# Performance work log

Hardware: AMD Instinct MI355X
Metric: run time of the kernel (lower is better)

Reference implementation:

```python
import jax, jax.numpy as jnp
import numpy as np

W = H = 64
CONFIGS = [(1, 3), (2, 3), (3, 3)]  # (dilation, kernel_size)
OUT_PER_CFG = 32
IN_CH = 32


def build_mask():
    # One (W+1, H+1) mask per config, broadcast over (out, in) channels.
    masks = []
    for d, k in CONFIGS:
        m = np.zeros((W + 1, H + 1), dtype=np.float32)
        k1 = (k - 1) * (d - 1) + k  # effective dilated kernel extent
        s1 = (W - k1) // 2 + 1
        e1 = (W + k1) // 2 + 1
        s2 = (H - k1) // 2 + 1
        e2 = (H + k1) // 2 + 1
        m[s1:e1:d, s2:e2:d] = 1.0
        masks.append(np.broadcast_to(m, (OUT_PER_CFG, 1, W + 1, H + 1)))
    return jnp.asarray(np.concatenate(masks, axis=0))  # (96, 1, 65, 65)


def setup_inputs() -> dict:
    key = jax.random.key(0)
    k1, k2 = jax.random.split(key)
    x = jax.random.normal(k1, (16, IN_CH, W, H), dtype=jnp.float32)
    # small init so tanh does not saturate
    weight = jax.random.normal(k2, (OUT_PER_CFG * len(CONFIGS), IN_CH, W + 1, H + 1), dtype=jnp.float32) * 0.01
    mask = build_mask()
    gamma = jnp.ones((OUT_PER_CFG * len(CONFIGS),), dtype=jnp.float32)
    beta = jnp.zeros((OUT_PER_CFG * len(CONFIGS),), dtype=jnp.float32)
    return {"x": x, "weight": weight, "mask": mask, "gamma": gamma, "beta": beta}


def reference(x, weight, mask, gamma, beta):
    # circular pad: last dim by H//2 each side, dim -2 by W//2 each side
    xp = jnp.pad(x, ((0, 0), (0, 0), (W // 2, W // 2), (H // 2, H // 2)), mode="wrap")
    y = jax.lax.conv_general_dilated(
        xp, weight * mask,
        window_strides=(1, 1), padding="VALID",
        dimension_numbers=("NCHW", "OIHW", "NCHW"),
    )  # (B, 96, 64, 64)
    # BatchNorm2d in training mode: batch statistics over (N, H, W), eps=1e-5
    mean = jnp.mean(y, axis=(0, 2, 3))
    var = jnp.var(y, axis=(0, 2, 3))
    yn = (y - mean[None, :, None, None]) * jax.lax.rsqrt(var + 1e-5)[None, :, None, None]
    yn = yn * gamma[None, :, None, None] + beta[None, :, None, None]
    return jnp.tanh(yn)
```

## Files before the change

### kernel.cpp

```cpp
#include <hip/hip_runtime.h>
#include <math.h>

#define BATCH 16
#define CIN 32
#define COUT 96
#define WH 64
#define IMG (WH*WH)
#define NPIX (BATCH*IMG)
#define PWELEMS (3*9*32*32)
#define XTELEMS (BATCH*IMG*CIN)
#define NBLK 768
#define NGRP 96
#define PAD 16
#define ZWORDS (4*NGRP*PAD + PAD)

typedef __attribute__((ext_vector_type(8))) short short8;
typedef __attribute__((ext_vector_type(4))) float floatx4;

__device__ __forceinline__ unsigned short f2bf(float f) {
    union { float f; unsigned u; } v; v.f = f;
    unsigned r = v.u + 0x7FFFu + ((v.u >> 16) & 1u);
    return (unsigned short)(r >> 16);
}
__device__ __forceinline__ float bf2f(unsigned short u) {
    union { unsigned u; float f; } v; v.u = (unsigned)u << 16; return v.f;
}

#define GLDS(src, dst) __builtin_amdgcn_global_load_lds( \
    (const __attribute__((address_space(1))) void*)(src), \
    (__attribute__((address_space(3))) void*)(dst), 16, 0, 0)

__device__ __forceinline__ float fast_tanh(float xv) {
    float e = __expf(2.0f * xv);
    return fmaf(-2.0f, __builtin_amdgcn_rcpf(e + 1.0f), 1.0f);
}

__global__ __launch_bounds__(256) void prep_kernel(
    const float* __restrict__ x, const float* __restrict__ w,
    unsigned short* __restrict__ xT, unsigned short* __restrict__ pw,
    unsigned* __restrict__ zbase)
{
    int blk = blockIdx.x;
    if (blk < 512) {
        int gid  = blk * 256 + threadIdx.x;
        int pt   = gid >> 1;
        int half = gid & 1;
        int b    = pt >> 12;
        int pix  = pt & 4095;
        const float* xb = x + ((size_t)b * CIN + half * 16) * IMG + pix;
        unsigned packed[8];
#pragma unroll
        for (int c2 = 0; c2 < 8; c2++) {
            unsigned short lo = f2bf(xb[(size_t)(2 * c2) * IMG]);
            unsigned short hi = f2bf(xb[(size_t)(2 * c2 + 1) * IMG]);
            packed[c2] = (unsigned)lo | ((unsigned)hi << 16);
        }
        uint4* dst = (uint4*)(xT + (size_t)pt * 32 + half * 16);
        dst[0] = make_uint4(packed[0], packed[1], packed[2], packed[3]);
        dst[1] = make_uint4(packed[4], packed[5], packed[6], packed[7]);
    } else if (blk < 620) {
        int e = (blk - 512) * 256 + threadIdx.x;
        if (e >= PWELEMS) return;
        int cfg = e / (9 * 1024);
        int rem = e % (9 * 1024);
        int tap = rem >> 10;
        int oc  = (rem >> 5) & 31;
        int c   = rem & 31;
        int d   = cfg + 1;
        int du  = tap / 3, dv = tap % 3;
        size_t idx = (((size_t)(cfg * 32 + oc) * CIN + c) * 65 + (32 + (du - 1) * d)) * 65
                     + (32 + (dv - 1) * d);
        pw[e] = f2bf(w[idx]);
    } else {
        for (int i = threadIdx.x; i < ZWORDS; i += 256) zbase[i] = 0u;
    }
}

__global__ __launch_bounds__(256, 3) void conv_bn_kernel(
    const unsigned short* __restrict__ xT, const unsigned short* __restrict__ pw,
    float* __restrict__ gsum, float* __restrict__ gsq,
    unsigned* __restrict__ gcnt, unsigned* __restrict__ ggo,
    unsigned* __restrict__ groot,
    const float* __restrict__ gamma, const float* __restrict__ beta,
    float* __restrict__ out)
{
    __shared__ __align__(16) unsigned short tile[10 * 2048];
    __shared__ float red_s[4][32];
    __shared__ float red_q[4][32];
    __shared__ float sc_a[32];
    __shared__ float sc_b[32];

    int bid  = blockIdx.x;
    int rowg = bid & 15;
    int rest = bid >> 4;
    int cfg  = rest % 3;
    int b    = rest / 3;
    int d    = cfg + 1;
    int i0   = rowg * 4;

    int t    = threadIdx.x;
    int wv   = t >> 6;
    int lane = t & 63;
    int l15  = lane & 15;
    int quad = lane >> 4;

    const unsigned short* xTb = xT + (size_t)b * IMG * 32;
#pragma unroll
    for (int rr = 0; rr < 10; rr++) {
        int gi = (i0 - 3 + rr) & 63;
        GLDS(xTb + (size_t)gi * 2048 + t * 8, &tile[rr * 2048 + t * 8]);
    }

    const unsigned short* pwc = pw + (size_t)cfg * 9 * 32 * 32;
    short8 af[2][9];
#pragma unroll
    for (int h = 0; h < 2; h++)
#pragma unroll
        for (int tap = 0; tap < 9; tap++)
            af[h][tap] = *(const short8*)(pwc + ((tap * 32 + h * 16 + l15) * 32 + quad * 8));

    float gam = 0.f, bet = 0.f;
    if (t < 32) { gam = gamma[cfg * 32 + t]; bet = beta[cfg * 32 + t]; }

    __syncthreads();

    float ss[2][4], qq[2][4];
#pragma unroll
    for (int h = 0; h < 2; h++)
#pragma unroll
        for (int r = 0; r < 4; r++) { ss[h][r] = 0.f; qq[h][r] = 0.f; }

    unsigned ypk[2][4][2];
    int row = i0 + wv;

#pragma unroll
    for (int cgi = 0; cgi < 4; cgi++) {
        floatx4 a0 = {0.f, 0.f, 0.f, 0.f};
        floatx4 a1 = {0.f, 0.f, 0.f, 0.f};
#pragma unroll
        for (int du = 0; du < 3; du++) {
            int rowloc = wv + 3 + (du - 1) * d;
            const unsigned short* rbase = &tile[rowloc * 2048 + quad * 8];
#pragma unroll
            for (int dv = 0; dv < 3; dv++) {
                int col = (cgi * 16 + l15 + (dv - 1) * d) & 63;
                short8 bf = *(const short8*)(rbase + col * 32);
                a0 = __builtin_amdgcn_mfma_f32_16x16x32_bf16(af[0][du * 3 + dv], bf, a0, 0, 0, 0);
                a1 = __builtin_amdgcn_mfma_f32_16x16x32_bf16(af[1][du * 3 + dv], bf, a1, 0, 0, 0);
            }
        }
#pragma unroll
        for (int r = 0; r < 4; r++) {
            float v0 = a0[r], v1 = a1[r];
            unsigned short h0 = f2bf(v0), h1 = f2bf(v1);
            if (cgi & 1) {
                ypk[0][r][cgi >> 1] |= (unsigned)h0 << 16;
                ypk[1][r][cgi >> 1] |= (unsigned)h1 << 16;
            } else {
                ypk[0][r][cgi >> 1] = (unsigned)h0;
                ypk[1][r][cgi >> 1] = (unsigned)h1;
            }
            ss[0][r] += v0; qq[0][r] = fmaf(v0, v0, qq[0][r]);
            ss[1][r] += v1; qq[1][r] = fmaf(v1, v1, qq[1][r]);
        }
    }

#pragma unroll
    for (int h = 0; h < 2; h++)
#pragma unroll
        for (int r = 0; r < 4; r++) {
            float s = ss[h][r], q = qq[h][r];
            for (int m = 1; m < 16; m <<= 1) {
                s += __shfl_xor(s, m, 64);
                q += __shfl_xor(q, m, 64);
            }
            if (l15 == 0) {
                red_s[wv][h * 16 + quad * 4 + r] = s;
                red_q[wv][h * 16 + quad * 4 + r] = q;
            }
        }
    __syncthreads();

    if (t < 32) {
        float S = red_s[0][t] + red_s[1][t] + red_s[2][t] + red_s[3][t];
        atomicAdd(&gsum[(cfg * 32 + t) * PAD], S);
    } else if (t < 64) {
        int o = t - 32;
        float Q = red_q[0][o] + red_q[1][o] + red_q[2][o] + red_q[3][o];
        atomicAdd(&gsq[(cfg * 32 + o) * PAD], Q);
    }
    __syncthreads();

    if (t == 0) {
        int g = bid >> 3;
        unsigned r = __hip_atomic_fetch_add(&gcnt[g * PAD], 1u,
                                            __ATOMIC_RELAXED, __HIP_MEMORY_SCOPE_AGENT);
        if (r == 7u) {
            unsigned rr = __hip_atomic_fetch_add(groot, 1u,
                                                 __ATOMIC_RELAXED, __HIP_MEMORY_SCOPE_AGENT);
            if (rr == (unsigned)(NGRP - 1)) {
                for (int gg = 0; gg < NGRP; gg++)
                    __hip_atomic_store(&ggo[gg * PAD], 1u,
                                       __ATOMIC_RELAXED, __HIP_MEMORY_SCOPE_AGENT);
            }
        }
        while (__hip_atomic_load(&ggo[g * PAD], __ATOMIC_RELAXED,
                                 __HIP_MEMORY_SCOPE_AGENT) == 0u)
            __builtin_amdgcn_s_sleep(4);
    }
    __syncthreads();

    if (t < 32) {
        int ch = cfg * 32 + t;
        float S = __hip_atomic_load(&gsum[ch * PAD], __ATOMIC_RELAXED, __HIP_MEMORY_SCOPE_AGENT);
        float Q = __hip_atomic_load(&gsq[ch * PAD],  __ATOMIC_RELAXED, __HIP_MEMORY_SCOPE_AGENT);
        const float inv_n = 1.0f / (float)NPIX;
        float mean = S * inv_n;
        float var  = Q * inv_n - mean * mean;
        float a    = gam * rsqrtf(var + 1e-5f);
        sc_a[t] = a;
        sc_b[t] = bet - mean * a;
    }
    __syncthreads();

#pragma unroll
    for (int h = 0; h < 2; h++)
#pragma unroll
        for (int r = 0; r < 4; r++) {
            int m0  = quad * 4 + r;
            int chl = h * 16 + m0;
            float a  = sc_a[chl];
            float bb = sc_b[chl];
            float* obase = out + ((size_t)b * COUT + cfg * 32 + chl) * IMG
                               + (size_t)row * WH + l15;
#pragma unroll
            for (int g = 0; g < 2; g++) {
                unsigned pk = ypk[h][r][g];
                obase[(2 * g) * 16]     = fast_tanh(fmaf(bf2f((unsigned short)(pk & 0xffffu)), a, bb));
                obase[(2 * g + 1) * 16] = fast_tanh(fmaf(bf2f((unsigned short)(pk >> 16)), a, bb));
            }
        }
}

extern "C" void kernel_launch(void* const* d_in, const int* in_sizes, int n_in,
                              void* d_out, int out_size, void* d_ws, size_t ws_size,
                              hipStream_t stream) {
    const float* x     = (const float*)d_in[0];
    const float* w     = (const float*)d_in[1];
    const float* gamma = (const float*)d_in[3];
    const float* beta  = (const float*)d_in[4];
    float* out = (float*)d_out;

    unsigned short* xT = (unsigned short*)d_ws;
    unsigned short* pw = xT + XTELEMS;
    float* gsum = (float*)(pw + PWELEMS + 32);
    float* gsq  = gsum + NGRP * PAD;
    unsigned* gcnt  = (unsigned*)(gsq + NGRP * PAD);
    unsigned* ggo   = gcnt + NGRP * PAD;
    unsigned* groot = ggo + NGRP * PAD;

    prep_kernel<<<621, 256, 0, stream>>>(x, w, xT, pw, (unsigned*)gsum);
    conv_bn_kernel<<<NBLK, 256, 0, stream>>>(xT, pw, gsum, gsq, gcnt, ggo, groot,
                                             gamma, beta, out);
}
```

Measured before the change: 116.0 us.

## Split grid barrier per config and remap blocks by XCD

Block indices are remapped so that consecutive blocks, which are dispatched round-robin across XCDs, map to batch images per XCD. The single global barrier becomes three independent per-config barriers, since each config's channels only need statistics from their own blocks. Blocks of one config can therefore proceed to normalization without waiting for the other configs, and the spin-wait sleep is shortened. The cost is three root counters instead of one and some extra index arithmetic.

```diff
diff --git a/kernel.cpp b/kernel.cpp
--- a/kernel.cpp
+++ b/kernel.cpp
@@ -12,7 +12,7 @@
 #define NBLK 768
 #define NGRP 96
 #define PAD 16
-#define ZWORDS (4*NGRP*PAD + PAD)
+#define ZWORDS (4*NGRP*PAD + 3*PAD)
 
 typedef __attribute__((ext_vector_type(8))) short short8;
 typedef __attribute__((ext_vector_type(4))) float floatx4;
@@ -80,7 +80,7 @@
     const unsigned short* __restrict__ xT, const unsigned short* __restrict__ pw,
     float* __restrict__ gsum, float* __restrict__ gsq,
     unsigned* __restrict__ gcnt, unsigned* __restrict__ ggo,
-    unsigned* __restrict__ groot,
+    unsigned* __restrict__ root,
     const float* __restrict__ gamma, const float* __restrict__ beta,
     float* __restrict__ out)
 {
@@ -91,12 +91,16 @@
     __shared__ float sc_b[32];
 
     int bid  = blockIdx.x;
-    int rowg = bid & 15;
-    int rest = bid >> 4;
-    int cfg  = rest % 3;
-    int b    = rest / 3;
+    int xcd  = bid & 7;
+    int idx  = bid >> 3;
+    int bsel = idx / 48;
+    int r48  = idx % 48;
+    int cfg  = r48 >> 4;
+    int rowg = r48 & 15;
+    int b    = xcd + 8 * bsel;
     int d    = cfg + 1;
     int i0   = rowg * 4;
+    int grp  = cfg * 32 + xcd * 4 + (rowg >> 2);
 
     int t    = threadIdx.x;
     int wv   = t >> 6;
@@ -192,21 +196,20 @@
     __syncthreads();
 
     if (t == 0) {
-        int g = bid >> 3;
-        unsigned r = __hip_atomic_fetch_add(&gcnt[g * PAD], 1u,
+        unsigned r = __hip_atomic_fetch_add(&gcnt[grp * PAD], 1u,
                                             __ATOMIC_RELAXED, __HIP_MEMORY_SCOPE_AGENT);
         if (r == 7u) {
-            unsigned rr = __hip_atomic_fetch_add(groot, 1u,
+            unsigned rr = __hip_atomic_fetch_add(&root[cfg * PAD], 1u,
                                                  __ATOMIC_RELAXED, __HIP_MEMORY_SCOPE_AGENT);
-            if (rr == (unsigned)(NGRP - 1)) {
-                for (int gg = 0; gg < NGRP; gg++)
+            if (rr == 31u) {
+                for (int gg = cfg * 32; gg < cfg * 32 + 32; gg++)
                     __hip_atomic_store(&ggo[gg * PAD], 1u,
                                        __ATOMIC_RELAXED, __HIP_MEMORY_SCOPE_AGENT);
             }
         }
-        while (__hip_atomic_load(&ggo[g * PAD], __ATOMIC_RELAXED,
+        while (__hip_atomic_load(&ggo[grp * PAD], __ATOMIC_RELAXED,
                                  __HIP_MEMORY_SCOPE_AGENT) == 0u)
-            __builtin_amdgcn_s_sleep(4);
+            __builtin_amdgcn_s_sleep(2);
     }
     __syncthreads();
 
@@ -255,11 +258,11 @@
     unsigned short* pw = xT + XTELEMS;
     float* gsum = (float*)(pw + PWELEMS + 32);
     float* gsq  = gsum + NGRP * PAD;
-    unsigned* gcnt  = (unsigned*)(gsq + NGRP * PAD);
-    unsigned* ggo   = gcnt + NGRP * PAD;
-    unsigned* groot = ggo + NGRP * PAD;
+    unsigned* gcnt = (unsigned*)(gsq + NGRP * PAD);
+    unsigned* ggo  = gcnt + NGRP * PAD;
+    unsigned* root = ggo + NGRP * PAD;
 
     prep_kernel<<<621, 256, 0, stream>>>(x, w, xT, pw, (unsigned*)gsum);
-    conv_bn_kernel<<<NBLK, 256, 0, stream>>>(xT, pw, gsum, gsq, gcnt, ggo, groot,
+    conv_bn_kernel<<<NBLK, 256, 0, stream>>>(xT, pw, gsum, gsq, gcnt, ggo, root,
                                              gamma, beta, out);
 }
```

After: 116.1 us. About the same (+0.1%).
